# Kernel tuning notes

Hardware: AMD Instinct MI355X
Metric: run time of the kernel (lower is better)

The kernel has to match this reference:

```python
import jax, jax.numpy as jnp
import numpy as np
from jax import lax

V, E, H, K, T = 100000, 256, 512, 16, 4096
START, END = 14, 15
NEG = -10000.0


def setup_inputs() -> dict:
    key = jax.random.key(0)
    ks = jax.random.split(key, 16)
    s = 1.0 / np.sqrt(H)
    u = lambda k, shp: jax.random.uniform(k, shp, jnp.float32, -s, s)
    x = jax.random.randint(ks[0], (1, T), 0, V)
    embed = 0.02 * jax.random.normal(ks[1], (V, E), jnp.float32)
    h0 = jax.random.normal(ks[2], (2, 1, H), jnp.float32)
    c0 = jax.random.normal(ks[3], (2, 1, H), jnp.float32)
    W_ih_f, W_hh_f = u(ks[4], (4 * H, E)), u(ks[5], (4 * H, H))
    b_f = u(ks[6], (4 * H,))
    W_ih_b, W_hh_b = u(ks[7], (4 * H, E)), u(ks[8], (4 * H, H))
    b_b = u(ks[9], (4 * H,))
    fc_w, fc_b = u(ks[10], (K, 2 * H)), u(ks[11], (K,))
    trans = jax.random.normal(ks[12], (K, K), jnp.float32)
    trans = trans.at[START, :].set(NEG).at[:, END].set(NEG)
    return {"x": x, "h0": h0, "c0": c0, "embed": embed,
            "W_ih_f": W_ih_f, "W_hh_f": W_hh_f, "b_f": b_f,
            "W_ih_b": W_ih_b, "W_hh_b": W_hh_b, "b_b": b_b,
            "fc_w": fc_w, "fc_b": fc_b, "transitions": trans}


def _lstm_dir(emb, h0, c0, Wih, Whh, b, reverse):
    # emb: [T, E]; PyTorch gate order i, f, g, o
    def step(carry, xt):
        h, c = carry
        g = xt @ Wih.T + h @ Whh.T + b  # [4H]
        i, f, gg, o = jnp.split(g, 4)
        c = jax.nn.sigmoid(f) * c + jax.nn.sigmoid(i) * jnp.tanh(gg)
        h = jax.nn.sigmoid(o) * jnp.tanh(c)
        return (h, c), h
    _, hs = lax.scan(step, (h0, c0), emb, reverse=reverse)
    return hs  # [T, H]


def reference(x, h0, c0, embed, W_ih_f, W_hh_f, b_f, W_ih_b, W_hh_b, b_b,
              fc_w, fc_b, transitions):
    emb = embed[x[0]]  # [T, E]
    hf = _lstm_dir(emb, h0[0, 0], c0[0, 0], W_ih_f, W_hh_f, b_f, False)
    hb = _lstm_dir(emb, h0[1, 0], c0[1, 0], W_ih_b, W_hh_b, b_b, True)
    lstm_out = jnp.concatenate([hf, hb], axis=-1)  # [T, 2H]
    feats = lstm_out @ fc_w.T + fc_b  # [T, K]

    # Viterbi DP: transitions[next, prev]
    v0 = jnp.full((K,), NEG, jnp.float32).at[START].set(0.0)
    def vit(v, feat):
        sc = v[None, :] + transitions  # [K_next, K_prev]
        return jnp.max(sc, axis=1) + feat, jnp.argmax(sc, axis=1)
    vT, bps = lax.scan(vit, v0, feats)  # bps: [T, K]
    term = vT + transitions[END]
    best = jnp.argmax(term)
    score = term[best]
    def back(tag, bp):
        return bp[tag], tag
    _, path = lax.scan(back, best, bps, reverse=True)  # [T]
    return score, path
```

## Files before the change

kernel.cpp:

```cpp
#include <hip/hip_runtime.h>
#include <hip/hip_bf16.h>

#define T_LEN 4096
#define HID   512
#define EMB   256
#define KTAG  16
#define START_TAG 14
#define END_TAG   15
#define NEGV  (-10000.0f)
#define NWG   64

__device__ __forceinline__ unsigned long long packph(float h, unsigned tag) {
  return ((unsigned long long)tag << 32) | (unsigned long long)__float_as_uint(h);
}

__global__ __launch_bounds__(256, 1) void lstm_kernel(
    const float* __restrict__ Whh_f, const float* __restrict__ Whh_b,
    const float* __restrict__ Wih_f, const float* __restrict__ Wih_b,
    const float* __restrict__ b_f,  const float* __restrict__ b_b,
    const float* __restrict__ h0,   const float* __restrict__ c0,
    const int*   __restrict__ x,    const float* __restrict__ embed,
    unsigned long long* __restrict__ pairs,
    float* __restrict__ hOut)
{
  const int wg   = blockIdx.x;
  const int dir  = wg >> 5;
  const int sl   = wg & 31;
  const int J0   = sl * 16;
  const int tid  = threadIdx.x;
  const int w    = tid >> 6;
  const int l    = tid & 63;
  const int jl   = l & 15;
  const int comp = J0 + jl;
  const int grow = (l >> 4) * HID + comp;

  const float* Whh = dir ? Whh_b : Whh_f;
  const float* Wih = dir ? Wih_b : Wih_f;
  const float* bb  = dir ? b_b  : b_f;

  float wh[128];
  {
    const float* wr = Whh + (size_t)grow * HID + w * 128;
    #pragma unroll
    for (int i = 0; i < 32; ++i)
      *(float4*)&wh[i*4] = *(const float4*)&wr[i*4];
  }
  float we[64];
  {
    const float* wr2 = Wih + (size_t)grow * EMB + w * 64;
    #pragma unroll
    for (int i = 0; i < 16; ++i)
      *(float4*)&we[i*4] = *(const float4*)&wr2[i*4];
  }
  const float bi = bb[comp],       bfg = bb[HID + comp];
  const float bg = bb[2*HID + comp], bo = bb[3*HID + comp];
  float c = c0[dir * HID + comp];

  __shared__ float hl[4][128];
  __shared__ float el[4][64];
  __shared__ float ps[2][4][64];

  unsigned long long* pb = pairs + (size_t)dir * 2 * 512;

  if (w == 0 && l < 16)
    __hip_atomic_store(&pb[512 + J0 + l], packph(h0[dir*HID + J0 + l], 1u),
                       __ATOMIC_RELAXED, __HIP_MEMORY_SCOPE_AGENT);

  float epf;
  {
    const int tt0 = dir ? (T_LEN - 1) : 0;
    epf = embed[(size_t)x[tt0] * EMB + w * 64 + l];
  }

  unsigned spins = 0;

  for (int t = 0; t < T_LEN; ++t) {
    const int par = t & 1;
    const int tt  = dir ? (T_LEN - 1 - t) : t;

    unsigned long long* psrc = pb + ((par ^ 1) * 512) + w * 128 + 2 * l;
    unsigned long long p0 = __hip_atomic_load(&psrc[0], __ATOMIC_RELAXED, __HIP_MEMORY_SCOPE_AGENT);
    unsigned long long p1 = __hip_atomic_load(&psrc[1], __ATOMIC_RELAXED, __HIP_MEMORY_SCOPE_AGENT);

    el[w][l] = epf;
    __builtin_amdgcn_wave_barrier();
    asm volatile("s_waitcnt lgkmcnt(0)" ::: "memory");
    __builtin_amdgcn_sched_barrier(0);

    float acc = 0.f;
    {
      const float* eseg = el[w];
      #pragma unroll
      for (int i = 0; i < 16; ++i) {
        float4 ev = *(const float4*)&eseg[i*4];
        acc += we[i*4+0]*ev.x + we[i*4+1]*ev.y + we[i*4+2]*ev.z + we[i*4+3]*ev.w;
      }
    }

    const unsigned tgt = (unsigned)(t + 1);
    for (;;) {
      bool f = ((unsigned)(p0 >> 32) == tgt) && ((unsigned)(p1 >> 32) == tgt);
      if (__all(f)) break;
      if (++spins > 2000000u) break;
      __builtin_amdgcn_s_sleep(1);
      p0 = __hip_atomic_load(&psrc[0], __ATOMIC_RELAXED, __HIP_MEMORY_SCOPE_AGENT);
      p1 = __hip_atomic_load(&psrc[1], __ATOMIC_RELAXED, __HIP_MEMORY_SCOPE_AGENT);
    }

    {
      float2 hv2;
      hv2.x = __uint_as_float((unsigned)p0);
      hv2.y = __uint_as_float((unsigned)p1);
      *(float2*)&hl[w][2*l] = hv2;
    }
    __builtin_amdgcn_wave_barrier();
    asm volatile("s_waitcnt lgkmcnt(0)" ::: "memory");
    __builtin_amdgcn_sched_barrier(0);

    {
      const float* hseg = hl[w];
      #pragma unroll
      for (int i = 0; i < 32; ++i) {
        float4 hv = *(const float4*)&hseg[i*4];
        acc += wh[i*4+0]*hv.x + wh[i*4+1]*hv.y + wh[i*4+2]*hv.z + wh[i*4+3]*hv.w;
      }
    }

    ps[par][w][l] = acc;
    __syncthreads();

    if (w == 0) {
      const float q0 = ps[par][0][l], q1 = ps[par][1][l];
      const float q2 = ps[par][2][l], q3 = ps[par][3][l];
      const float tot = (q0 + q1) + (q2 + q3);
      const float g0 = __shfl(tot, jl);
      const float g1 = __shfl(tot, jl + 16);
      const float g2 = __shfl(tot, jl + 32);
      const float g3 = __shfl(tot, jl + 48);
      const float gi_ = g0 + bi, gf_ = g1 + bfg, gg_ = g2 + bg, go_ = g3 + bo;
      const float si = 1.f / (1.f + expf(-gi_));
      const float sf = 1.f / (1.f + expf(-gf_));
      const float so = 1.f / (1.f + expf(-go_));
      const float cn = sf * c + si * tanhf(gg_);
      c = cn;
      const float hv = so * tanhf(cn);
      if (l < 16) {
        __hip_atomic_store(&pb[par * 512 + J0 + l], packph(hv, (unsigned)(t + 2)),
                           __ATOMIC_RELAXED, __HIP_MEMORY_SCOPE_AGENT);
        hOut[((size_t)dir * T_LEN + tt) * HID + J0 + l] = hv;
      }
    }

    if (t + 1 < T_LEN) {
      const int ttn = dir ? (T_LEN - 2 - t) : (t + 1);
      epf = embed[(size_t)x[ttn] * EMB + w * 64 + l];
    }
  }
}

__global__ __launch_bounds__(256) void feats_kernel(
    const float* __restrict__ hOut, const float* __restrict__ fc_w,
    const float* __restrict__ fc_b, float* __restrict__ feats)
{
  const int tid = threadIdx.x;
  const int k   = tid & 15;
  const int tl  = tid >> 4;
  const int t   = blockIdx.x * 16 + tl;
  const float* hf = hOut + (size_t)t * HID;
  const float* hb = hOut + ((size_t)T_LEN + t) * HID;
  const float* wr = fc_w + (size_t)k * (2 * HID);
  float acc = fc_b[k];
  #pragma unroll 4
  for (int j = 0; j < HID; j += 4) {
    float4 hv = *(const float4*)&hf[j];
    float4 wv = *(const float4*)&wr[j];
    acc += hv.x*wv.x + hv.y*wv.y + hv.z*wv.z + hv.w*wv.w;
  }
  #pragma unroll 4
  for (int j = 0; j < HID; j += 4) {
    float4 hv = *(const float4*)&hb[j];
    float4 wv = *(const float4*)&wr[HID + j];
    acc += hv.x*wv.x + hv.y*wv.y + hv.z*wv.z + hv.w*wv.w;
  }
  feats[(size_t)t * KTAG + k] = acc;
}

__global__ __launch_bounds__(256) void viterbi_kernel(
    const float* __restrict__ feats, const float* __restrict__ trans,
    float* __restrict__ out)
{
  __shared__ float fch[256 * KTAG];
  __shared__ unsigned char bps8[T_LEN * 8];
  __shared__ float vl[KTAG];
  __shared__ unsigned char ml[64 * 16];
  __shared__ unsigned char rb[64];
  __shared__ int sbest;

  const int tid  = threadIdx.x;
  const int lane = tid & 63;
  const int nxt  = lane >> 2;
  const int pg   = lane & 3;

  float tr[4];
  if (tid < 64) {
    #pragma unroll
    for (int p = 0; p < 4; ++p)
      tr[p] = trans[nxt * KTAG + pg * 4 + p];
  }
  if (tid < KTAG) vl[tid] = (tid == START_TAG) ? 0.f : NEGV;
  __syncthreads();

  for (int ch = 0; ch < 16; ++ch) {
    const float* src = feats + (size_t)ch * 256 * KTAG;
    #pragma unroll
    for (int i = 0; i < 4; ++i)
      *(float4*)&fch[(i * 256 + tid) * 4] = *(const float4*)&src[(i * 256 + tid) * 4];
    __syncthreads();

    if (tid < 64) {
      for (int tl = 0; tl < 256; ++tl) {
        const int t = ch * 256 + tl;
        float best = -3.0e38f; int bp = 0;
        #pragma unroll
        for (int p = 0; p < 4; ++p) {
          const float sc = vl[pg * 4 + p] + tr[p];
          if (sc > best) { best = sc; bp = pg * 4 + p; }
        }
        #pragma unroll
        for (int m = 1; m <= 2; m <<= 1) {
          const float ob = __shfl_xor(best, m);
          const int  obp = __shfl_xor(bp, m);
          if (ob > best || (ob == best && obp < bp)) { best = ob; bp = obp; }
        }
        const int nbp = __shfl(bp, (lane + 4) & 63);
        if (pg == 0) {
          if ((nxt & 1) == 0)
            bps8[t * 8 + (nxt >> 1)] = (unsigned char)(bp | (nbp << 4));
          vl[nxt] = best + fch[tl * KTAG + nxt];
        }
      }
    }
    __syncthreads();
  }

  if (tid < 64) {
    float term = (lane < KTAG) ? (vl[lane] + trans[END_TAG * KTAG + lane]) : -3.0e38f;
    int bt = (lane < KTAG) ? lane : KTAG;
    #pragma unroll
    for (int m = 1; m < 64; m <<= 1) {
      const float ot = __shfl_xor(term, m);
      const int  obt = __shfl_xor(bt, m);
      if (ot > term || (ot == term && obt < bt)) { term = ot; bt = obt; }
    }
    if (lane == 0) { out[0] = term; sbest = bt; }
  }
  __syncthreads();

  if (tid < 64) {
    const int L = lane;
    unsigned char cur[16];
    #pragma unroll
    for (int g = 0; g < 16; ++g) cur[g] = (unsigned char)g;
    for (int i = 63; i >= 0; --i) {
      const int t = L * 64 + i;
      #pragma unroll
      for (int g = 0; g < 16; ++g) {
        const unsigned char cc = cur[g];
        const unsigned char by = bps8[t * 8 + (cc >> 1)];
        cur[g] = (cc & 1) ? (by >> 4) : (by & 15);
      }
    }
    #pragma unroll
    for (int g = 0; g < 16; ++g) ml[L * 16 + g] = cur[g];
  }
  __syncthreads();

  if (tid == 0) {
    int r = sbest;
    rb[63] = (unsigned char)r;
    for (int cix = 62; cix >= 0; --cix) {
      r = ml[(cix + 1) * 16 + r];
      rb[cix] = (unsigned char)r;
    }
  }
  __syncthreads();

  if (tid < 64) {
    const int L = lane;
    int tag = rb[L];
    out[1 + L * 64 + 63] = (float)tag;
    for (int i = 62; i >= 0; --i) {
      const int t = L * 64 + i + 1;
      const unsigned char by = bps8[t * 8 + (tag >> 1)];
      tag = (tag & 1) ? (by >> 4) : (by & 15);
      out[1 + L * 64 + i] = (float)tag;
    }
  }
}

extern "C" void kernel_launch(void* const* d_in, const int* in_sizes, int n_in,
                              void* d_out, int out_size, void* d_ws, size_t ws_size,
                              hipStream_t stream) {
  (void)in_sizes; (void)n_in; (void)out_size; (void)ws_size;
  const int*   x      = (const int*)  d_in[0];
  const float* h0     = (const float*)d_in[1];
  const float* c0     = (const float*)d_in[2];
  const float* embed  = (const float*)d_in[3];
  const float* Wih_f  = (const float*)d_in[4];
  const float* Whh_f  = (const float*)d_in[5];
  const float* b_f    = (const float*)d_in[6];
  const float* Wih_b  = (const float*)d_in[7];
  const float* Whh_b  = (const float*)d_in[8];
  const float* b_b    = (const float*)d_in[9];
  const float* fc_w   = (const float*)d_in[10];
  const float* fc_b   = (const float*)d_in[11];
  const float* trans  = (const float*)d_in[12];
  float* out = (float*)d_out;

  char* ws = (char*)d_ws;
  unsigned long long* pairs = (unsigned long long*)(ws + 0);
  float* feats    = (float*)(ws + 65536);
  float* hOut     = (float*)(ws + (1ull << 20));

  hipMemsetAsync(pairs, 0, 2 * 2 * 512 * sizeof(unsigned long long), stream);

  {
    void* args[] = {
      (void*)&Whh_f, (void*)&Whh_b, (void*)&Wih_f, (void*)&Wih_b,
      (void*)&b_f,   (void*)&b_b,   (void*)&h0,    (void*)&c0,
      (void*)&x,     (void*)&embed, (void*)&pairs, (void*)&hOut
    };
    hipLaunchCooperativeKernel((const void*)lstm_kernel, dim3(NWG), dim3(256),
                               args, 0, stream);
  }

  feats_kernel<<<dim3(T_LEN / 16), 256, 0, stream>>>(hOut, fc_w, fc_b, feats);
  viterbi_kernel<<<dim3(1), 256, 0, stream>>>(feats, trans, out);
}
```

Measured before the change: 10.47 ms.

## Co-locate LSTM workgroups on one XCC and use sc0 loads for h exchange

Launches 256 workgroups, reads each one's XCC id, elects the most populated XCC and claims 32 team slots there, so all recurrent workers share one L2. When placement is uniform and a handshake succeeds, h exchange uses sc0 global loads and stores without sleeps; otherwise it falls back to agent-scope atomics. Each workgroup now computes 32 hidden units instead of 16, doubling register-held weights while halving the team size. Viterbi keeps its state in registers and uses shuffles instead of LDS. The added election protocol brings launch overhead and relies on sc0 coherence within one XCC.

```diff
diff --git a/kernel.cpp b/kernel.cpp
--- a/kernel.cpp
+++ b/kernel.cpp
@@ -8,10 +8,193 @@
 #define START_TAG 14
 #define END_TAG   15
 #define NEGV  (-10000.0f)
-#define NWG   64
+#define NTEAM   32
+#define NLAUNCH 256
+
+#define E_CENSUS 0
+#define E_ARRIVE 8
+#define E_CHOSEN 9
+#define E_CLAIM  10
+#define E_VOTE   12
+#define E_XCC    16
+
+typedef __attribute__((ext_vector_type(4))) unsigned int uint4v;
 
 __device__ __forceinline__ unsigned long long packph(float h, unsigned tag) {
   return ((unsigned long long)tag << 32) | (unsigned long long)__float_as_uint(h);
+}
+
+__device__ __forceinline__ void issue_ld4_sc0(const unsigned long long* p, uint4v& d) {
+  asm volatile("global_load_dwordx4 %0, %1, off sc0" : "=&v"(d) : "v"(p));
+}
+__device__ __forceinline__ void wait_ld(uint4v& d) {
+  asm volatile("s_waitcnt vmcnt(0)" : "+v"(d) :: "memory");
+}
+__device__ __forceinline__ void st_pair_sc0(unsigned long long* p, unsigned long long v) {
+  asm volatile("global_store_dwordx2 %0, %1, off sc0" :: "v"(p), "v"(v) : "memory");
+}
+__device__ __forceinline__ unsigned long long ld_pair_agent(const unsigned long long* p) {
+  return __hip_atomic_load(p, __ATOMIC_RELAXED, __HIP_MEMORY_SCOPE_AGENT);
+}
+__device__ __forceinline__ void st_pair_agent(unsigned long long* p, unsigned long long v) {
+  __hip_atomic_store(p, v, __ATOMIC_RELAXED, __HIP_MEMORY_SCOPE_AGENT);
+}
+
+template<int FAST>
+__device__ void lstm_body(
+    const float* __restrict__ Whh, const float* __restrict__ Wih,
+    const float* __restrict__ bb,  const float* __restrict__ c0,
+    const int*   __restrict__ x,   const float* __restrict__ embed,
+    unsigned long long* __restrict__ pb, float* __restrict__ hOut,
+    int dir, int sl, int w, int l)
+{
+  const int J0   = sl * 32;
+  const int jl   = l & 15;
+  const int gate = l >> 4;
+  const int r0   = gate * HID + J0 + jl;
+  const int r1   = r0 + 16;
+
+  float wh0[128], wh1[128], we0[64], we1[64];
+  {
+    const float* p0 = Whh + (size_t)r0 * HID + w * 128;
+    const float* p1 = Whh + (size_t)r1 * HID + w * 128;
+    #pragma unroll
+    for (int i = 0; i < 32; ++i) {
+      *(float4*)&wh0[i*4] = *(const float4*)&p0[i*4];
+      *(float4*)&wh1[i*4] = *(const float4*)&p1[i*4];
+    }
+    const float* q0 = Wih + (size_t)r0 * EMB + w * 64;
+    const float* q1 = Wih + (size_t)r1 * EMB + w * 64;
+    #pragma unroll
+    for (int i = 0; i < 16; ++i) {
+      *(float4*)&we0[i*4] = *(const float4*)&q0[i*4];
+      *(float4*)&we1[i*4] = *(const float4*)&q1[i*4];
+    }
+  }
+  const int ac = J0 + (l & 31);
+  const float bi = bb[ac], bfg = bb[HID + ac];
+  const float bg = bb[2*HID + ac], bo = bb[3*HID + ac];
+  float cst = c0[dir * HID + ac];
+
+  __shared__ float hl[4][128];
+  __shared__ float el[4][64];
+  __shared__ float ps[2][4][2][64];
+
+  float epf;
+  {
+    const int tt0 = dir ? (T_LEN - 1) : 0;
+    epf = embed[(size_t)x[tt0] * EMB + w * 64 + l];
+  }
+
+  unsigned spins = 0;
+
+  for (int t = 0; t < T_LEN; ++t) {
+    const int par = t & 1;
+    const int tt  = dir ? (T_LEN - 1 - t) : t;
+
+    unsigned long long* psrc = pb + ((par ^ 1) * 512) + w * 128 + 2 * l;
+    uint4v fpr;
+    unsigned long long sp0 = 0, sp1 = 0;
+    if (FAST) {
+      issue_ld4_sc0(psrc, fpr);
+    } else {
+      sp0 = ld_pair_agent(&psrc[0]);
+      sp1 = ld_pair_agent(&psrc[1]);
+    }
+
+    el[w][l] = epf;
+    __builtin_amdgcn_wave_barrier();
+    asm volatile("s_waitcnt lgkmcnt(0)" ::: "memory");
+    __builtin_amdgcn_sched_barrier(0);
+
+    float acc0 = 0.f, acc1 = 0.f;
+    {
+      const float* eseg = el[w];
+      #pragma unroll
+      for (int i = 0; i < 16; ++i) {
+        float4 ev = *(const float4*)&eseg[i*4];
+        acc0 += we0[i*4+0]*ev.x + we0[i*4+1]*ev.y + we0[i*4+2]*ev.z + we0[i*4+3]*ev.w;
+        acc1 += we1[i*4+0]*ev.x + we1[i*4+1]*ev.y + we1[i*4+2]*ev.z + we1[i*4+3]*ev.w;
+      }
+    }
+
+    const unsigned tgt = (unsigned)(t + 1);
+    if (FAST) {
+      wait_ld(fpr);
+      for (;;) {
+        if (__all((fpr.y == tgt) && (fpr.w == tgt))) break;
+        if (++spins > 4000000u) break;
+        issue_ld4_sc0(psrc, fpr);
+        wait_ld(fpr);
+      }
+    } else {
+      for (;;) {
+        const bool f = ((unsigned)(sp0 >> 32) == tgt) && ((unsigned)(sp1 >> 32) == tgt);
+        if (__all(f)) break;
+        if (++spins > 4000000u) break;
+        __builtin_amdgcn_s_sleep(1);
+        sp0 = ld_pair_agent(&psrc[0]);
+        sp1 = ld_pair_agent(&psrc[1]);
+      }
+    }
+
+    {
+      float2 hv2;
+      if (FAST) { hv2.x = __uint_as_float(fpr.x); hv2.y = __uint_as_float(fpr.z); }
+      else      { hv2.x = __uint_as_float((unsigned)sp0); hv2.y = __uint_as_float((unsigned)sp1); }
+      *(float2*)&hl[w][2*l] = hv2;
+    }
+    __builtin_amdgcn_wave_barrier();
+    asm volatile("s_waitcnt lgkmcnt(0)" ::: "memory");
+    __builtin_amdgcn_sched_barrier(0);
+
+    {
+      const float* hseg = hl[w];
+      #pragma unroll
+      for (int i = 0; i < 32; ++i) {
+        float4 hv = *(const float4*)&hseg[i*4];
+        acc0 += wh0[i*4+0]*hv.x + wh0[i*4+1]*hv.y + wh0[i*4+2]*hv.z + wh0[i*4+3]*hv.w;
+        acc1 += wh1[i*4+0]*hv.x + wh1[i*4+1]*hv.y + wh1[i*4+2]*hv.z + wh1[i*4+3]*hv.w;
+      }
+    }
+
+    ps[par][w][0][l] = acc0;
+    ps[par][w][1][l] = acc1;
+    __syncthreads();
+
+    if (w == 0) {
+      const float t0 = (ps[par][0][0][l] + ps[par][1][0][l])
+                     + (ps[par][2][0][l] + ps[par][3][0][l]);
+      const float t1 = (ps[par][0][1][l] + ps[par][1][1][l])
+                     + (ps[par][2][1][l] + ps[par][3][1][l]);
+      const float a0 = __shfl(t0, jl),      b0 = __shfl(t1, jl);
+      const float a1 = __shfl(t0, 16 + jl), b1 = __shfl(t1, 16 + jl);
+      const float a2 = __shfl(t0, 32 + jl), b2 = __shfl(t1, 32 + jl);
+      const float a3 = __shfl(t0, 48 + jl), b3 = __shfl(t1, 48 + jl);
+      if (l < 32) {
+        const bool hi = (l & 16) != 0;
+        const float gi_ = (hi ? b0 : a0) + bi;
+        const float gf_ = (hi ? b1 : a1) + bfg;
+        const float gg_ = (hi ? b2 : a2) + bg;
+        const float go_ = (hi ? b3 : a3) + bo;
+        const float si = 1.f / (1.f + expf(-gi_));
+        const float sf = 1.f / (1.f + expf(-gf_));
+        const float so = 1.f / (1.f + expf(-go_));
+        const float cn = sf * cst + si * tanhf(gg_);
+        cst = cn;
+        const float hv = so * tanhf(cn);
+        const unsigned long long pk = packph(hv, (unsigned)(t + 2));
+        if (FAST) st_pair_sc0(&pb[par * 512 + J0 + l], pk);
+        else      st_pair_agent(&pb[par * 512 + J0 + l], pk);
+        hOut[((size_t)dir * T_LEN + tt) * HID + J0 + l] = hv;
+      }
+    }
+
+    if (t + 1 < T_LEN) {
+      const int ttn = dir ? (T_LEN - 2 - t) : (t + 1);
+      epf = embed[(size_t)x[ttn] * EMB + w * 64 + l];
+    }
+  }
 }
 
 __global__ __launch_bounds__(256, 1) void lstm_kernel(
@@ -21,141 +204,115 @@
     const float* __restrict__ h0,   const float* __restrict__ c0,
     const int*   __restrict__ x,    const float* __restrict__ embed,
     unsigned long long* __restrict__ pairs,
-    float* __restrict__ hOut)
+    unsigned long long* __restrict__ pairs2,
+    float* __restrict__ hOut, int* __restrict__ elect)
 {
-  const int wg   = blockIdx.x;
-  const int dir  = wg >> 5;
-  const int sl   = wg & 31;
-  const int J0   = sl * 16;
-  const int tid  = threadIdx.x;
-  const int w    = tid >> 6;
-  const int l    = tid & 63;
-  const int jl   = l & 15;
-  const int comp = J0 + jl;
-  const int grow = (l >> 4) * HID + comp;
+  const int tid = threadIdx.x;
+  __shared__ int s_slot, s_mode;
+  __shared__ int s_ok[4];
+
+  if (tid == 0) {
+    int xcc;
+    asm volatile("s_getreg_b32 %0, hwreg(HW_REG_XCC_ID)" : "=s"(xcc));
+    xcc &= 7;
+    __hip_atomic_fetch_add(&elect[E_CENSUS + xcc], 1, __ATOMIC_RELAXED, __HIP_MEMORY_SCOPE_AGENT);
+    const int a = __hip_atomic_fetch_add(&elect[E_ARRIVE], 1, __ATOMIC_ACQ_REL, __HIP_MEMORY_SCOPE_AGENT);
+    if (a == NLAUNCH - 1) {
+      int best = 0, bc = -1;
+      for (int i = 0; i < 8; ++i) {
+        const int ci = __hip_atomic_load(&elect[E_CENSUS + i], __ATOMIC_RELAXED, __HIP_MEMORY_SCOPE_AGENT);
+        if (ci > bc) { bc = ci; best = i; }
+      }
+      __hip_atomic_store(&elect[E_CHOSEN], best + 1, __ATOMIC_RELEASE, __HIP_MEMORY_SCOPE_AGENT);
+    }
+    int ch = 0;
+    for (unsigned g = 0; g < 300000u; ++g) {
+      ch = __hip_atomic_load(&elect[E_CHOSEN], __ATOMIC_ACQUIRE, __HIP_MEMORY_SCOPE_AGENT);
+      if (ch) break;
+      __builtin_amdgcn_s_sleep(2);
+    }
+    int slot = -1;
+    if (ch == 0 || ch - 1 == xcc) {
+      const int cl = __hip_atomic_fetch_add(&elect[E_CLAIM], 1, __ATOMIC_RELAXED, __HIP_MEMORY_SCOPE_AGENT);
+      if (cl < NTEAM) slot = cl;
+    }
+    if (slot >= 0)
+      __hip_atomic_store(&elect[E_XCC + slot], xcc + 1, __ATOMIC_RELEASE, __HIP_MEMORY_SCOPE_AGENT);
+    s_slot = slot;
+  }
+  __syncthreads();
+  const int slot = s_slot;
+  if (slot < 0) return;
+
+  const int dir = slot >> 4;
+  const int sl  = slot & 15;
+  const int J0  = sl * 32;
+  const int w   = tid >> 6;
+  const int l   = tid & 63;
+
+  if (tid == 0) {
+    int uni = 0;
+    for (unsigned g = 0; g < 60000u; ++g) {
+      int allnz = 1;
+      for (int i = 0; i < NTEAM; ++i)
+        if (!__hip_atomic_load(&elect[E_XCC + i], __ATOMIC_ACQUIRE, __HIP_MEMORY_SCOPE_AGENT)) { allnz = 0; break; }
+      if (allnz) { uni = 1; break; }
+      __builtin_amdgcn_s_sleep(2);
+    }
+    if (uni) {
+      const int v0 = __hip_atomic_load(&elect[E_XCC], __ATOMIC_RELAXED, __HIP_MEMORY_SCOPE_AGENT);
+      for (int i = 1; i < NTEAM; ++i)
+        if (__hip_atomic_load(&elect[E_XCC + i], __ATOMIC_RELAXED, __HIP_MEMORY_SCOPE_AGENT) != v0) { uni = 0; break; }
+    }
+    s_mode = uni;
+  }
+  __syncthreads();
+
+  if (s_mode) {
+    if (w == 0 && l < 32)
+      st_pair_sc0(&pairs[(size_t)dir * 1024 + 512 + J0 + l],
+                  packph(h0[dir * HID + J0 + l], 1u));
+    int okw = 0;
+    {
+      const unsigned long long* hp = pairs + (size_t)dir * 1024 + 512 + w * 128 + 2 * l;
+      uint4v pr;
+      for (unsigned g = 0; g < 50000u; ++g) {
+        issue_ld4_sc0(hp, pr);
+        wait_ld(pr);
+        if (__all((pr.y == 1u) && (pr.w == 1u))) { okw = 1; break; }
+      }
+    }
+    if (l == 0) s_ok[w] = okw;
+    __syncthreads();
+    if (tid == 0) {
+      const int ok = s_ok[0] & s_ok[1] & s_ok[2] & s_ok[3];
+      __hip_atomic_fetch_add(&elect[E_VOTE], ok ? 1 : 0x10000, __ATOMIC_ACQ_REL, __HIP_MEMORY_SCOPE_AGENT);
+      int v = 0;
+      for (unsigned g = 0; g < 300000u; ++g) {
+        v = __hip_atomic_load(&elect[E_VOTE], __ATOMIC_ACQUIRE, __HIP_MEMORY_SCOPE_AGENT);
+        if ((v & 0xffff) + (v >> 16) >= NTEAM) break;
+        __builtin_amdgcn_s_sleep(2);
+      }
+      s_mode = ((v >> 16) == 0 && (v & 0xffff) >= NTEAM) ? 1 : 0;
+    }
+    __syncthreads();
+  }
+  const int mode = s_mode;
+
+  if (!mode) {
+    if (w == 0 && l < 32)
+      st_pair_agent(&pairs2[(size_t)dir * 1024 + 512 + J0 + l],
+                    packph(h0[dir * HID + J0 + l], 1u));
+  }
 
   const float* Whh = dir ? Whh_b : Whh_f;
   const float* Wih = dir ? Wih_b : Wih_f;
   const float* bb  = dir ? b_b  : b_f;
 
-  float wh[128];
-  {
-    const float* wr = Whh + (size_t)grow * HID + w * 128;
-    #pragma unroll
-    for (int i = 0; i < 32; ++i)
-      *(float4*)&wh[i*4] = *(const float4*)&wr[i*4];
-  }
-  float we[64];
-  {
-    const float* wr2 = Wih + (size_t)grow * EMB + w * 64;
-    #pragma unroll
-    for (int i = 0; i < 16; ++i)
-      *(float4*)&we[i*4] = *(const float4*)&wr2[i*4];
-  }
-  const float bi = bb[comp],       bfg = bb[HID + comp];
-  const float bg = bb[2*HID + comp], bo = bb[3*HID + comp];
-  float c = c0[dir * HID + comp];
-
-  __shared__ float hl[4][128];
-  __shared__ float el[4][64];
-  __shared__ float ps[2][4][64];
-
-  unsigned long long* pb = pairs + (size_t)dir * 2 * 512;
-
-  if (w == 0 && l < 16)
-    __hip_atomic_store(&pb[512 + J0 + l], packph(h0[dir*HID + J0 + l], 1u),
-                       __ATOMIC_RELAXED, __HIP_MEMORY_SCOPE_AGENT);
-
-  float epf;
-  {
-    const int tt0 = dir ? (T_LEN - 1) : 0;
-    epf = embed[(size_t)x[tt0] * EMB + w * 64 + l];
-  }
-
-  unsigned spins = 0;
-
-  for (int t = 0; t < T_LEN; ++t) {
-    const int par = t & 1;
-    const int tt  = dir ? (T_LEN - 1 - t) : t;
-
-    unsigned long long* psrc = pb + ((par ^ 1) * 512) + w * 128 + 2 * l;
-    unsigned long long p0 = __hip_atomic_load(&psrc[0], __ATOMIC_RELAXED, __HIP_MEMORY_SCOPE_AGENT);
-    unsigned long long p1 = __hip_atomic_load(&psrc[1], __ATOMIC_RELAXED, __HIP_MEMORY_SCOPE_AGENT);
-
-    el[w][l] = epf;
-    __builtin_amdgcn_wave_barrier();
-    asm volatile("s_waitcnt lgkmcnt(0)" ::: "memory");
-    __builtin_amdgcn_sched_barrier(0);
-
-    float acc = 0.f;
-    {
-      const float* eseg = el[w];
-      #pragma unroll
-      for (int i = 0; i < 16; ++i) {
-        float4 ev = *(const float4*)&eseg[i*4];
-        acc += we[i*4+0]*ev.x + we[i*4+1]*ev.y + we[i*4+2]*ev.z + we[i*4+3]*ev.w;
-      }
-    }
-
-    const unsigned tgt = (unsigned)(t + 1);
-    for (;;) {
-      bool f = ((unsigned)(p0 >> 32) == tgt) && ((unsigned)(p1 >> 32) == tgt);
-      if (__all(f)) break;
-      if (++spins > 2000000u) break;
-      __builtin_amdgcn_s_sleep(1);
-      p0 = __hip_atomic_load(&psrc[0], __ATOMIC_RELAXED, __HIP_MEMORY_SCOPE_AGENT);
-      p1 = __hip_atomic_load(&psrc[1], __ATOMIC_RELAXED, __HIP_MEMORY_SCOPE_AGENT);
-    }
-
-    {
-      float2 hv2;
-      hv2.x = __uint_as_float((unsigned)p0);
-      hv2.y = __uint_as_float((unsigned)p1);
-      *(float2*)&hl[w][2*l] = hv2;
-    }
-    __builtin_amdgcn_wave_barrier();
-    asm volatile("s_waitcnt lgkmcnt(0)" ::: "memory");
-    __builtin_amdgcn_sched_barrier(0);
-
-    {
-      const float* hseg = hl[w];
-      #pragma unroll
-      for (int i = 0; i < 32; ++i) {
-        float4 hv = *(const float4*)&hseg[i*4];
-        acc += wh[i*4+0]*hv.x + wh[i*4+1]*hv.y + wh[i*4+2]*hv.z + wh[i*4+3]*hv.w;
-      }
-    }
-
-    ps[par][w][l] = acc;
-    __syncthreads();
-
-    if (w == 0) {
-      const float q0 = ps[par][0][l], q1 = ps[par][1][l];
-      const float q2 = ps[par][2][l], q3 = ps[par][3][l];
-      const float tot = (q0 + q1) + (q2 + q3);
-      const float g0 = __shfl(tot, jl);
-      const float g1 = __shfl(tot, jl + 16);
-      const float g2 = __shfl(tot, jl + 32);
-      const float g3 = __shfl(tot, jl + 48);
-      const float gi_ = g0 + bi, gf_ = g1 + bfg, gg_ = g2 + bg, go_ = g3 + bo;
-      const float si = 1.f / (1.f + expf(-gi_));
-      const float sf = 1.f / (1.f + expf(-gf_));
-      const float so = 1.f / (1.f + expf(-go_));
-      const float cn = sf * c + si * tanhf(gg_);
-      c = cn;
-      const float hv = so * tanhf(cn);
-      if (l < 16) {
-        __hip_atomic_store(&pb[par * 512 + J0 + l], packph(hv, (unsigned)(t + 2)),
-                           __ATOMIC_RELAXED, __HIP_MEMORY_SCOPE_AGENT);
-        hOut[((size_t)dir * T_LEN + tt) * HID + J0 + l] = hv;
-      }
-    }
-
-    if (t + 1 < T_LEN) {
-      const int ttn = dir ? (T_LEN - 2 - t) : (t + 1);
-      epf = embed[(size_t)x[ttn] * EMB + w * 64 + l];
-    }
-  }
+  if (mode)
+    lstm_body<1>(Whh, Wih, bb, c0, x, embed, pairs  + (size_t)dir * 1024, hOut, dir, sl, w, l);
+  else
+    lstm_body<0>(Whh, Wih, bb, c0, x, embed, pairs2 + (size_t)dir * 1024, hOut, dir, sl, w, l);
 }
 
 __global__ __launch_bounds__(256) void feats_kernel(
@@ -191,7 +348,6 @@
 {
   __shared__ float fch[256 * KTAG];
   __shared__ unsigned char bps8[T_LEN * 8];
-  __shared__ float vl[KTAG];
   __shared__ unsigned char ml[64 * 16];
   __shared__ unsigned char rb[64];
   __shared__ int sbest;
@@ -201,13 +357,13 @@
   const int nxt  = lane >> 2;
   const int pg   = lane & 3;
 
-  float tr[4];
+  float tr[4] = {0.f, 0.f, 0.f, 0.f};
   if (tid < 64) {
     #pragma unroll
     for (int p = 0; p < 4; ++p)
       tr[p] = trans[nxt * KTAG + pg * 4 + p];
   }
-  if (tid < KTAG) vl[tid] = (tid == START_TAG) ? 0.f : NEGV;
+  float vlreg = ((lane >> 2) == START_TAG) ? 0.f : NEGV;
   __syncthreads();
 
   for (int ch = 0; ch < 16; ++ch) {
@@ -218,14 +374,17 @@
     __syncthreads();
 
     if (tid < 64) {
+      const int sbase = pg << 4;
       for (int tl = 0; tl < 256; ++tl) {
         const int t = ch * 256 + tl;
-        float best = -3.0e38f; int bp = 0;
-        #pragma unroll
-        for (int p = 0; p < 4; ++p) {
-          const float sc = vl[pg * 4 + p] + tr[p];
-          if (sc > best) { best = sc; bp = pg * 4 + p; }
-        }
+        const float s0 = __shfl(vlreg, sbase);
+        const float s1 = __shfl(vlreg, sbase + 4);
+        const float s2 = __shfl(vlreg, sbase + 8);
+        const float s3 = __shfl(vlreg, sbase + 12);
+        float best = s0 + tr[0]; int bp = pg * 4;
+        float sc = s1 + tr[1]; if (sc > best) { best = sc; bp = pg * 4 + 1; }
+        sc = s2 + tr[2]; if (sc > best) { best = sc; bp = pg * 4 + 2; }
+        sc = s3 + tr[3]; if (sc > best) { best = sc; bp = pg * 4 + 3; }
         #pragma unroll
         for (int m = 1; m <= 2; m <<= 1) {
           const float ob = __shfl_xor(best, m);
@@ -233,18 +392,18 @@
           if (ob > best || (ob == best && obp < bp)) { best = ob; bp = obp; }
         }
         const int nbp = __shfl(bp, (lane + 4) & 63);
-        if (pg == 0) {
-          if ((nxt & 1) == 0)
-            bps8[t * 8 + (nxt >> 1)] = (unsigned char)(bp | (nbp << 4));
-          vl[nxt] = best + fch[tl * KTAG + nxt];
-        }
+        if (pg == 0 && (nxt & 1) == 0)
+          bps8[t * 8 + (nxt >> 1)] = (unsigned char)(bp | (nbp << 4));
+        const float fv = fch[tl * KTAG + nxt];
+        vlreg = (pg == 0) ? (best + fv) : vlreg;
       }
     }
     __syncthreads();
   }
 
   if (tid < 64) {
-    float term = (lane < KTAG) ? (vl[lane] + trans[END_TAG * KTAG + lane]) : -3.0e38f;
+    const float vfin = __shfl(vlreg, (lane & 15) << 2);
+    float term = (lane < KTAG) ? (vfin + trans[END_TAG * KTAG + lane]) : -3.0e38f;
     int bt = (lane < KTAG) ? lane : KTAG;
     #pragma unroll
     for (int m = 1; m < 64; m <<= 1) {
@@ -318,19 +477,22 @@
   float* out = (float*)d_out;
 
   char* ws = (char*)d_ws;
-  unsigned long long* pairs = (unsigned long long*)(ws + 0);
+  unsigned long long* pairs  = (unsigned long long*)(ws + 0);
+  unsigned long long* pairs2 = (unsigned long long*)(ws + 16384);
+  int*   elect    = (int*)(ws + 32768);
   float* feats    = (float*)(ws + 65536);
   float* hOut     = (float*)(ws + (1ull << 20));
 
-  hipMemsetAsync(pairs, 0, 2 * 2 * 512 * sizeof(unsigned long long), stream);
+  hipMemsetAsync(ws, 0, 36864, stream);
 
   {
     void* args[] = {
       (void*)&Whh_f, (void*)&Whh_b, (void*)&Wih_f, (void*)&Wih_b,
       (void*)&b_f,   (void*)&b_b,   (void*)&h0,    (void*)&c0,
-      (void*)&x,     (void*)&embed, (void*)&pairs, (void*)&hOut
+      (void*)&x,     (void*)&embed, (void*)&pairs, (void*)&pairs2,
+      (void*)&hOut,  (void*)&elect
     };
-    hipLaunchCooperativeKernel((const void*)lstm_kernel, dim3(NWG), dim3(256),
+    hipLaunchCooperativeKernel((const void*)lstm_kernel, dim3(NLAUNCH), dim3(256),
                                args, 0, stream);
   }
 
```

Result: slower. 18.86 ms (+80.1%).
